# Kernel tuning notes

Measured on AMD Instinct MI355X. Metric: run time of the kernel, lower is better.

Reference implementation:

```python
import jax, jax.numpy as jnp
import numpy as np

H_FEATS = 256
N_NODES = 100000
N_EDGES = 1000000
EDGE_FEAT_DIM = 7
OUT_DIM = 4


def setup_inputs() -> dict:
    key = jax.random.key(0)
    ks = jax.random.split(key, 8)
    h = jax.random.normal(ks[0], (N_NODES, H_FEATS), dtype=jnp.float32)
    edge_feat = jax.random.normal(ks[1], (N_EDGES, EDGE_FEAT_DIM), dtype=jnp.float32)
    src = jax.random.randint(ks[2], (N_EDGES,), 0, N_NODES, dtype=jnp.int64)
    dst = jax.random.randint(ks[3], (N_EDGES,), 0, N_NODES, dtype=jnp.int64)
    in_dim = 2 * H_FEATS + EDGE_FEAT_DIM  # 519
    # Kaiming-ish init scale for the linear layers
    W1_w = jax.random.normal(ks[4], (in_dim, H_FEATS), dtype=jnp.float32) / np.sqrt(in_dim)
    W1_b = jax.random.normal(ks[5], (H_FEATS,), dtype=jnp.float32) * 0.01
    W2_w = jax.random.normal(ks[6], (H_FEATS, OUT_DIM), dtype=jnp.float32) / np.sqrt(H_FEATS)
    W2_b = jax.random.normal(ks[7], (OUT_DIM,), dtype=jnp.float32) * 0.01
    return {"h": h, "edge_feat": edge_feat, "src": src, "dst": dst,
            "W1_w": W1_w, "W1_b": W1_b, "W2_w": W2_w, "W2_b": W2_b}


def reference(h, edge_feat, src, dst, W1_w, W1_b, W2_w, W2_b):
    # Gather src/dst node embeddings per edge, concat with edge features: [E, 2*h_feats+7]
    x = jnp.concatenate([edge_feat, h[src], h[dst]], axis=1)
    # 2-layer MLP per edge: Linear -> ReLU -> Linear
    hid = jax.nn.relu(x @ W1_w + W1_b)          # [E, h_feats]
    rep = hid @ W2_w + W2_b                     # [E, 4]
    return rep
```

## Files before the change

### kernel.cpp

```cpp
#include <hip/hip_runtime.h>
#include <stdint.h>

#define NODES 100000
#define EDGES 1000000
#define HF 256
#define TILES2 (EDGES / 32)


typedef short short8 __attribute__((ext_vector_type(8)));
typedef float f32x4 __attribute__((ext_vector_type(4)));
typedef float f32x2 __attribute__((ext_vector_type(2)));
typedef int i32x4 __attribute__((ext_vector_type(4)));

__device__ __forceinline__ unsigned short f2b(float f) {
  union { float f; uint32_t u; } v; v.f = f;
  return (unsigned short)((v.u + 0x7FFFu + ((v.u >> 16) & 1u)) >> 16);
}
__device__ __forceinline__ float asf(uint32_t u) {
  union { uint32_t u; float f; } v; v.u = u;
  return v.f;
}
__device__ __forceinline__ uint32_t cvtpk(float lo, float hi) {
  uint32_t pk;
  asm("v_cvt_pk_bf16_f32 %0, %1, %2" : "=v"(pk) : "v"(lo), "v"(hi));
  return pk;
}

__global__ __launch_bounds__(256) void pack_w1(const float* __restrict__ W1,
                                               unsigned short* __restrict__ Bp) {
  int idx = blockIdx.x * 256 + threadIdx.x;
  int lane = idx & 63;
  int nbg  = (idx >> 6) & 31;
  int kb   = idx >> 11;
  int n    = nbg * 16 + (lane & 15);
  int k0   = kb * 32 + (lane >> 4) * 8;
  int rbase = (n < 256) ? 7 : 263;
  int col   = n & 255;
  short8 o;
#pragma unroll
  for (int j = 0; j < 8; ++j)
    o[j] = (short)f2b(W1[(size_t)(rbase + k0 + j) * HF + col]);
  *reinterpret_cast<short8*>(Bp + (size_t)idx * 8) = o;
}

__global__ __launch_bounds__(256) void gemm_R(const float* __restrict__ h,
                                              const unsigned short* __restrict__ Bp,
                                              const float* __restrict__ b1,
                                              unsigned short* __restrict__ R) {
  __shared__ unsigned short A[64][264];
  const int m0 = blockIdx.x * 64;
  const int t  = threadIdx.x;
  {
    const int r = t >> 2, q = t & 3;
    const int grow = m0 + r;
    const bool valid = grow < NODES;
    const float* hp = h + (size_t)grow * HF + q * 64;
#pragma unroll
    for (int cc = 0; cc < 8; ++cc) {
      float4 a, b;
      if (valid) {
        a = *reinterpret_cast<const float4*>(hp + cc * 8);
        b = *reinterpret_cast<const float4*>(hp + cc * 8 + 4);
      } else {
        a = make_float4(0.f, 0.f, 0.f, 0.f);
        b = a;
      }
      uint32_t o32[4];
      o32[0] = cvtpk(a.x, a.y);
      o32[1] = cvtpk(a.z, a.w);
      o32[2] = cvtpk(b.x, b.y);
      o32[3] = cvtpk(b.z, b.w);
      *reinterpret_cast<uint4*>(&A[r][q * 64 + cc * 8]) =
          make_uint4(o32[0], o32[1], o32[2], o32[3]);
    }
  }
  __syncthreads();

  const int wave = t >> 6, lane = t & 63;
  const int l15 = lane & 15, lhi = lane >> 4;
  const int nbg0 = blockIdx.y * 16 + wave * 4;
  f32x4 acc[4][4] = {};
#pragma unroll
  for (int kb = 0; kb < 8; ++kb) {
    short8 bfrag[4];
#pragma unroll
    for (int nb = 0; nb < 4; ++nb)
      bfrag[nb] = *reinterpret_cast<const short8*>(
          Bp + (((size_t)(kb * 32 + nbg0 + nb) * 64 + lane) * 8));
    short8 afrag[4];
#pragma unroll
    for (int mb = 0; mb < 4; ++mb)
      afrag[mb] = *reinterpret_cast<const short8*>(&A[mb * 16 + l15][kb * 32 + lhi * 8]);
#pragma unroll
    for (int mb = 0; mb < 4; ++mb)
#pragma unroll
      for (int nb = 0; nb < 4; ++nb)
        acc[mb][nb] = __builtin_amdgcn_mfma_f32_16x16x32_bf16(
            afrag[mb], bfrag[nb], acc[mb][nb], 0, 0, 0);
  }
  const int c0 = blockIdx.y * 256 + wave * 64 + l15;
  float b1v[4] = {0.f, 0.f, 0.f, 0.f};
  if (blockIdx.y == 0) {
#pragma unroll
    for (int nb = 0; nb < 4; ++nb) b1v[nb] = b1[c0 + nb * 16];
  }
#pragma unroll
  for (int mb = 0; mb < 4; ++mb) {
#pragma unroll
    for (int i = 0; i < 4; ++i) {
      const int row = m0 + mb * 16 + lhi * 4 + i;
      if (row < NODES) {
        unsigned short* rp = R + (size_t)row * 512 + c0;
#pragma unroll
        for (int nb = 0; nb < 4; ++nb) rp[nb * 16] = f2b(acc[mb][nb][i] + b1v[nb]);
      }
    }
  }
}

__global__ __launch_bounds__(256) void edge_mlp(
    const unsigned short* __restrict__ R, const float* __restrict__ ef,
    const int* __restrict__ src, const int* __restrict__ dst,
    const float* __restrict__ W1, const float* __restrict__ W2,
    const float* __restrict__ b2, float* __restrict__ out) {
  __shared__ float w1a[7 * 256];
  for (int i = threadIdx.x; i < 7 * 64; i += 256)
    reinterpret_cast<float4*>(w1a)[i] = reinterpret_cast<const float4*>(W1)[i];
  __syncthreads();

  const int lane = threadIdx.x & 63;
  const int l15 = lane & 15, lhi = lane >> 4;

  short8 bfrag[8];
#pragma unroll
  for (int kb = 0; kb < 8; ++kb) {
    short8 b = {0, 0, 0, 0, 0, 0, 0, 0};
    if (l15 < 4) {
#pragma unroll
      for (int j = 0; j < 8; ++j)
        b[j] = (short)f2b(W2[(size_t)(kb * 32 + lhi * 8 + j) * 4 + l15]);
    }
    bfrag[kb] = b;
  }
  const float b2l = (l15 < 4) ? b2[l15] : 0.f;

  const int wid = (blockIdx.x * blockDim.x + threadIdx.x) >> 6;
  const int nw  = (gridDim.x * blockDim.x) >> 6;

#define TILE_KB(PV, QV, EFV, ACC)                                              \
  {                                                                            \
    const uint32_t* pu = reinterpret_cast<const uint32_t*>(&PV);               \
    const uint32_t* qu = reinterpret_cast<const uint32_t*>(&QV);               \
    f32x2 hd[4];                                                               \
    _Pragma("unroll") for (int w = 0; w < 4; ++w) {                            \
      f32x2 p2 = {asf(pu[w] << 16), asf(pu[w] & 0xffff0000u)};                 \
      f32x2 q2 = {asf(qu[w] << 16), asf(qu[w] & 0xffff0000u)};                 \
      hd[w] = p2 + q2;                                                         \
    }                                                                          \
    _Pragma("unroll") for (int j = 0; j < 7; ++j) {                            \
      f32x2 e2 = {EFV[j], EFV[j]};                                             \
      hd[0] = wv[j][0] * e2 + hd[0];                                           \
      hd[1] = wv[j][1] * e2 + hd[1];                                           \
      hd[2] = wv[j][2] * e2 + hd[2];                                           \
      hd[3] = wv[j][3] * e2 + hd[3];                                           \
    }                                                                          \
    union { i32x4 i; short8 s8; } af;                                          \
    _Pragma("unroll") for (int w = 0; w < 4; ++w) {                            \
      const float lo = fmaxf(hd[w][0], 0.f);                                   \
      const float hi = fmaxf(hd[w][1], 0.f);                                   \
      af.i[w] = (int)cvtpk(lo, hi);                                            \
    }                                                                          \
    ACC = __builtin_amdgcn_mfma_f32_16x16x32_bf16(af.s8, bfrag[kb], ACC, 0, 0, 0); \
  }

  for (int t = wid; t < TILES2; t += nw) {
    const int e0 = t * 32;
    const int eiA = e0 + l15;
    const int eiB = eiA + 16;
    const int sA = src[eiA], dA = dst[eiA];
    const int sB = src[eiB], dB = dst[eiB];
    float efA[7], efB[7];
#pragma unroll
    for (int j = 0; j < 7; ++j) {
      efA[j] = ef[(size_t)eiA * 7 + j];
      efB[j] = ef[(size_t)eiB * 7 + j];
    }
    const unsigned short* PpA = R + (size_t)sA * 512 + lhi * 8;
    const unsigned short* QpA = R + (size_t)dA * 512 + 256 + lhi * 8;
    const unsigned short* PpB = R + (size_t)sB * 512 + lhi * 8;
    const unsigned short* QpB = R + (size_t)dB * 512 + 256 + lhi * 8;

    short8 pA[8], qA[8], pB[8], qB[8];
#pragma unroll
    for (int kb = 0; kb < 2; ++kb) {
      pA[kb] = *reinterpret_cast<const short8*>(PpA + kb * 32);
      qA[kb] = *reinterpret_cast<const short8*>(QpA + kb * 32);
      pB[kb] = *reinterpret_cast<const short8*>(PpB + kb * 32);
      qB[kb] = *reinterpret_cast<const short8*>(QpB + kb * 32);
    }

    f32x4 accA = {}, accB = {};
#pragma unroll
    for (int kb = 0; kb < 8; ++kb) {
      if (kb < 6) {
        pA[kb + 2] = *reinterpret_cast<const short8*>(PpA + (kb + 2) * 32);
        qA[kb + 2] = *reinterpret_cast<const short8*>(QpA + (kb + 2) * 32);
        pB[kb + 2] = *reinterpret_cast<const short8*>(PpB + (kb + 2) * 32);
        qB[kb + 2] = *reinterpret_cast<const short8*>(QpB + (kb + 2) * 32);
      }
      f32x2 wv[7][4];
      const float* ws = w1a + kb * 32 + lhi * 8;
#pragma unroll
      for (int j = 0; j < 7; ++j) {
        const float4 wa = *reinterpret_cast<const float4*>(ws + j * 256);
        const float4 wb = *reinterpret_cast<const float4*>(ws + j * 256 + 4);
        wv[j][0] = {wa.x, wa.y};
        wv[j][1] = {wa.z, wa.w};
        wv[j][2] = {wb.x, wb.y};
        wv[j][3] = {wb.z, wb.w};
      }
      TILE_KB(pA[kb], qA[kb], efA, accA);
      TILE_KB(pB[kb], qB[kb], efB, accB);
    }
    if (l15 < 4) {
#pragma unroll
      for (int i = 0; i < 4; ++i) {
        out[(size_t)(e0 + lhi * 4 + i) * 4 + l15] = accA[i] + b2l;
        out[(size_t)(e0 + 16 + lhi * 4 + i) * 4 + l15] = accB[i] + b2l;
      }
    }
  }
#undef TILE_KB
}

extern "C" void kernel_launch(void* const* d_in, const int* in_sizes, int n_in,
                              void* d_out, int out_size, void* d_ws, size_t ws_size,
                              hipStream_t stream) {
  const float* h  = (const float*)d_in[0];
  const float* ef = (const float*)d_in[1];
  const int* src  = (const int*)d_in[2];
  const int* dst  = (const int*)d_in[3];
  const float* W1 = (const float*)d_in[4];
  const float* b1 = (const float*)d_in[5];
  const float* W2 = (const float*)d_in[6];
  const float* b2 = (const float*)d_in[7];
  float* out = (float*)d_out;

  const size_t bp_bytes = (size_t)8 * 32 * 64 * 8 * 2;
  unsigned short* Bp = (unsigned short*)d_ws;
  unsigned short* R  = (unsigned short*)((char*)d_ws + bp_bytes);

  pack_w1<<<64, 256, 0, stream>>>(W1, Bp);
  gemm_R<<<dim3((NODES + 63) / 64, 2), 256, 0, stream>>>(h, Bp, b1, R);
  edge_mlp<<<2048, 256, 0, stream>>>(R, ef, src, dst, W1, W2, b2, out);
}
```

Before: 239.9 us.

## Coalesce edge gathers with lane remap via bpermute and merge gemm_R column blocks

The edge MLP now gives each group of four lanes one edge, so the four 16-byte loads of a row segment sit next to each other in memory. The values are then moved back into MFMA fragment layout with ds_bpermute. The intent is better coalescing of the random R gathers, paid for by four extra cross-lane permutes per k-block. Separately, gemm_R drops the two-block grid in y: each block now computes all 512 output columns, reusing its A tile and h loads once instead of twice. That doubles the accumulator registers and sets launch_bounds to one block.

```diff
diff --git a/kernel.cpp b/kernel.cpp
--- a/kernel.cpp
+++ b/kernel.cpp
@@ -43,10 +43,10 @@
   *reinterpret_cast<short8*>(Bp + (size_t)idx * 8) = o;
 }
 
-__global__ __launch_bounds__(256) void gemm_R(const float* __restrict__ h,
-                                              const unsigned short* __restrict__ Bp,
-                                              const float* __restrict__ b1,
-                                              unsigned short* __restrict__ R) {
+__global__ __launch_bounds__(256, 1) void gemm_R(const float* __restrict__ h,
+                                                 const unsigned short* __restrict__ Bp,
+                                                 const float* __restrict__ b1,
+                                                 unsigned short* __restrict__ R) {
   __shared__ unsigned short A[64][264];
   const int m0 = blockIdx.x * 64;
   const int t  = threadIdx.x;
@@ -78,13 +78,13 @@
 
   const int wave = t >> 6, lane = t & 63;
   const int l15 = lane & 15, lhi = lane >> 4;
-  const int nbg0 = blockIdx.y * 16 + wave * 4;
-  f32x4 acc[4][4] = {};
+  const int nbg0 = wave * 8;
+  f32x4 acc[4][8] = {};
 #pragma unroll
   for (int kb = 0; kb < 8; ++kb) {
-    short8 bfrag[4];
-#pragma unroll
-    for (int nb = 0; nb < 4; ++nb)
+    short8 bfrag[8];
+#pragma unroll
+    for (int nb = 0; nb < 8; ++nb)
       bfrag[nb] = *reinterpret_cast<const short8*>(
           Bp + (((size_t)(kb * 32 + nbg0 + nb) * 64 + lane) * 8));
     short8 afrag[4];
@@ -94,15 +94,15 @@
 #pragma unroll
     for (int mb = 0; mb < 4; ++mb)
 #pragma unroll
-      for (int nb = 0; nb < 4; ++nb)
+      for (int nb = 0; nb < 8; ++nb)
         acc[mb][nb] = __builtin_amdgcn_mfma_f32_16x16x32_bf16(
             afrag[mb], bfrag[nb], acc[mb][nb], 0, 0, 0);
   }
-  const int c0 = blockIdx.y * 256 + wave * 64 + l15;
-  float b1v[4] = {0.f, 0.f, 0.f, 0.f};
-  if (blockIdx.y == 0) {
-#pragma unroll
-    for (int nb = 0; nb < 4; ++nb) b1v[nb] = b1[c0 + nb * 16];
+  const int c0 = wave * 128 + l15;
+  float b1v[8] = {};
+  if (wave < 2) {
+#pragma unroll
+    for (int nb = 0; nb < 8; ++nb) b1v[nb] = b1[c0 + nb * 16];
   }
 #pragma unroll
   for (int mb = 0; mb < 4; ++mb) {
@@ -112,7 +112,7 @@
       if (row < NODES) {
         unsigned short* rp = R + (size_t)row * 512 + c0;
 #pragma unroll
-        for (int nb = 0; nb < 4; ++nb) rp[nb * 16] = f2b(acc[mb][nb][i] + b1v[nb]);
+        for (int nb = 0; nb < 8; ++nb) rp[nb * 16] = f2b(acc[mb][nb][i] + b1v[nb]);
       }
     }
   }
@@ -130,6 +130,9 @@
 
   const int lane = threadIdx.x & 63;
   const int l15 = lane & 15, lhi = lane >> 4;
+  const int esub = lane >> 2;
+  const int sub  = lane & 3;
+  const int bperm_idx = ((((lane & 15) << 2) | (lane >> 4)) << 2);
 
   short8 bfrag[8];
 #pragma unroll
@@ -164,18 +167,18 @@
       hd[2] = wv[j][2] * e2 + hd[2];                                           \
       hd[3] = wv[j][3] * e2 + hd[3];                                           \
     }                                                                          \
-    union { i32x4 i; short8 s8; } af;                                          \
+    union { i32x4 i; short8 s8; } afm;                                         \
     _Pragma("unroll") for (int w = 0; w < 4; ++w) {                            \
       const float lo = fmaxf(hd[w][0], 0.f);                                   \
       const float hi = fmaxf(hd[w][1], 0.f);                                   \
-      af.i[w] = (int)cvtpk(lo, hi);                                            \
+      afm.i[w] = __builtin_amdgcn_ds_bpermute(bperm_idx, (int)cvtpk(lo, hi));  \
     }                                                                          \
-    ACC = __builtin_amdgcn_mfma_f32_16x16x32_bf16(af.s8, bfrag[kb], ACC, 0, 0, 0); \
+    ACC = __builtin_amdgcn_mfma_f32_16x16x32_bf16(afm.s8, bfrag[kb], ACC, 0, 0, 0); \
   }
 
   for (int t = wid; t < TILES2; t += nw) {
     const int e0 = t * 32;
-    const int eiA = e0 + l15;
+    const int eiA = e0 + esub;
     const int eiB = eiA + 16;
     const int sA = src[eiA], dA = dst[eiA];
     const int sB = src[eiB], dB = dst[eiB];
@@ -185,10 +188,10 @@
       efA[j] = ef[(size_t)eiA * 7 + j];
       efB[j] = ef[(size_t)eiB * 7 + j];
     }
-    const unsigned short* PpA = R + (size_t)sA * 512 + lhi * 8;
-    const unsigned short* QpA = R + (size_t)dA * 512 + 256 + lhi * 8;
-    const unsigned short* PpB = R + (size_t)sB * 512 + lhi * 8;
-    const unsigned short* QpB = R + (size_t)dB * 512 + 256 + lhi * 8;
+    const unsigned short* PpA = R + (size_t)sA * 512 + sub * 8;
+    const unsigned short* QpA = R + (size_t)dA * 512 + 256 + sub * 8;
+    const unsigned short* PpB = R + (size_t)sB * 512 + sub * 8;
+    const unsigned short* QpB = R + (size_t)dB * 512 + 256 + sub * 8;
 
     short8 pA[8], qA[8], pB[8], qB[8];
 #pragma unroll
@@ -209,7 +212,7 @@
         qB[kb + 2] = *reinterpret_cast<const short8*>(QpB + (kb + 2) * 32);
       }
       f32x2 wv[7][4];
-      const float* ws = w1a + kb * 32 + lhi * 8;
+      const float* ws = w1a + kb * 32 + sub * 8;
 #pragma unroll
       for (int j = 0; j < 7; ++j) {
         const float4 wa = *reinterpret_cast<const float4*>(ws + j * 256);
@@ -251,6 +254,6 @@
   unsigned short* R  = (unsigned short*)((char*)d_ws + bp_bytes);
 
   pack_w1<<<64, 256, 0, stream>>>(W1, Bp);
-  gemm_R<<<dim3((NODES + 63) / 64, 2), 256, 0, stream>>>(h, Bp, b1, R);
+  gemm_R<<<(NODES + 63) / 64, 256, 0, stream>>>(h, Bp, b1, R);
   edge_mlp<<<2048, 256, 0, stream>>>(R, ef, src, dst, W1, W2, b2, out);
 }
```

Result: no change. 236.6 us (-1.4%).
